# Kernel optimization log

Measured on AMD Instinct MI355X. Metric: run time of the kernel, lower is better.

The kernel has to match this reference:

```python
import jax, jax.numpy as jnp
import numpy as np

W_SEG = 2048   # segment length w
R = 4          # dilation rate
OFFSET = 0     # offset < r
H = 16         # num heads
C = 1024       # embed dim
M = W_SEG // R # tokens attended per segment


def _mha(xi, w_in, b_in, w_out, b_out):
    # xi: (b, s, m, c) -> causal multi-head self-attention per segment
    b, s, m, c = xi.shape
    dh = c // H
    qkv = jnp.einsum('bsmc,ec->bsme', xi, w_in) + b_in  # e = 3c
    q, k, v = jnp.split(qkv, 3, axis=-1)
    q = q.reshape(b, s, m, H, dh)
    k = k.reshape(b, s, m, H, dh)
    v = v.reshape(b, s, m, H, dh)
    scores = jnp.einsum('bsqhd,bskhd->bshqk', q, k) / jnp.sqrt(jnp.asarray(dh, xi.dtype))
    causal = jnp.tril(jnp.ones((m, m), dtype=bool))
    scores = jnp.where(causal, scores, jnp.asarray(-1e9, xi.dtype))
    p = jax.nn.softmax(scores, axis=-1)
    o = jnp.einsum('bshqk,bskhd->bsqhd', p, v).reshape(b, s, m, c)
    return jnp.einsum('bsmc,oc->bsmo', o, w_out) + b_out


def setup_inputs() -> dict:
    key = jax.random.key(0)
    k1, k2, k3, k4, k5 = jax.random.split(key, 5)
    x = jax.random.normal(k1, (4, 8192, C), dtype=jnp.float32)
    w_in = jax.random.normal(k2, (3 * C, C), dtype=jnp.float32) * (C ** -0.5)
    b_in = jnp.zeros((3 * C,), dtype=jnp.float32)
    w_out = jax.random.normal(k3, (C, C), dtype=jnp.float32) * (C ** -0.5)
    b_out = jnp.zeros((C,), dtype=jnp.float32)
    return {"x": x, "w_in": w_in, "b_in": b_in, "w_out": w_out, "b_out": b_out}


def reference(x, w_in, b_in, w_out, b_out):
    b, n, c = x.shape
    s = n // W_SEG  # number of segments
    xr = x.reshape(b, s, W_SEG, c)
    xi = xr[:, :, OFFSET::R, :]                # (b, s, m, c) dilated gather
    oi = _mha(xi, w_in, b_in, w_out, b_out)    # attention per segment
    out = jnp.zeros_like(xr).at[:, :, OFFSET::R, :].set(oi)  # scatter (disjoint indices)
    return out.reshape(b, n, c)
```

## Files before the change

kernel.cpp:

```cpp
#include <hip/hip_runtime.h>


typedef unsigned short u16;
typedef short short8 __attribute__((ext_vector_type(8)));
typedef short short4v __attribute__((ext_vector_type(4)));
typedef float f32x4 __attribute__((ext_vector_type(4)));

__device__ __forceinline__ u16 f2bf(float f) {
  unsigned u = __builtin_bit_cast(unsigned, f);
  u += 0x7FFFu + ((u >> 16) & 1u);
  return (u16)(u >> 16);
}

__device__ __forceinline__ void gload_lds16(const void* g, void* l) {
  __builtin_amdgcn_global_load_lds((const __attribute__((address_space(1))) void*)g,
                                   (__attribute__((address_space(3))) void*)l,
                                   16, 0, 0);
}

#define SBAR() asm volatile("s_barrier" ::: "memory")

__global__ void conv_gather(const float* __restrict__ x, u16* __restrict__ xi) {
  int t = blockIdx.x * 256 + threadIdx.x;
  if (t >= (8192 * 1024) / 8) return;
  int row = t >> 7;
  int col = (t & 127) << 3;
  size_t src = ((size_t)((row >> 9) << 11) + ((row & 511) << 2)) * 1024 + col;
  float4 v0 = *(const float4*)(x + src);
  float4 v1 = *(const float4*)(x + src + 4);
  short8 o;
  o[0] = f2bf(v0.x); o[1] = f2bf(v0.y); o[2] = f2bf(v0.z); o[3] = f2bf(v0.w);
  o[4] = f2bf(v1.x); o[5] = f2bf(v1.y); o[6] = f2bf(v1.z); o[7] = f2bf(v1.w);
  *(short8*)(xi + (size_t)row * 1024 + col) = o;
}

__global__ void conv_plain(const float* __restrict__ in, u16* __restrict__ out, int n8) {
  int t = blockIdx.x * 256 + threadIdx.x;
  if (t >= n8) return;
  size_t base = (size_t)t * 8;
  float4 v0 = *(const float4*)(in + base);
  float4 v1 = *(const float4*)(in + base + 4);
  short8 o;
  o[0] = f2bf(v0.x); o[1] = f2bf(v0.y); o[2] = f2bf(v0.z); o[3] = f2bf(v0.w);
  o[4] = f2bf(v1.x); o[5] = f2bf(v1.y); o[6] = f2bf(v1.z); o[7] = f2bf(v1.w);
  *(short8*)(out + base) = o;
}

template <int NCOLS, int MODE>
__global__ __launch_bounds__(512) void gemm_pipe(
    const u16* __restrict__ A, const u16* __restrict__ B,
    const float* __restrict__ bias, void* __restrict__ Cout) {
  constexpr int K = 1024, NT = 16, NTILE = NCOLS / 256;
  __shared__ u16 lds[3][24576];

  const int tid = threadIdx.x;
  const int w = tid >> 6, lane = tid & 63;
  const int wm = w >> 2, wn = w & 3;
  const int g = lane >> 4, lq = lane & 15;

  const int per = gridDim.x >> 3;
  const int s = (blockIdx.x & 7) * per + (blockIdx.x >> 3);
  const int m0 = (s / NTILE) * 128, n0 = (s % NTILE) * 256;

  const int srow = w * 8 + (lane >> 3);
  const int jch = (lane & 7) ^ ((lane >> 3) & 7);
  const u16* Ab = A + (size_t)(m0 + srow) * K + jch * 8;
  const u16* Bb = B + (size_t)(n0 + srow) * K + jch * 8;
  const int ldst = w * 512 + lane * 8;

#define SA(buf_, qd, kt) gload_lds16(Ab + (size_t)(qd) * 64 * K + (kt) * 64, &lds[buf_][(qd) * 4096 + ldst])
#define SB(buf_, qd, kt) gload_lds16(Bb + (size_t)(qd) * 64 * K + (kt) * 64, &lds[buf_][8192 + (qd) * 4096 + ldst])
#define STAGE6(kt)                                                                 \
  { const int nb_ = (kt) % 3;                                                      \
    SA(nb_, 0, kt); SA(nb_, 1, kt);                                                \
    SB(nb_, 0, kt); SB(nb_, 1, kt); SB(nb_, 2, kt); SB(nb_, 3, kt); }

  const int xw = lq & 7;
  const int arow = wm * 64 + lq;
  const int brow = wn * 64 + lq;

#define READ_TILE(aset, bset, tile_)                                               \
  { const int bufr = (tile_) % 3;                                                  \
    _Pragma("unroll") for (int kc = 0; kc < 2; ++kc) {                             \
      _Pragma("unroll") for (int mi = 0; mi < 4; ++mi)                             \
        aset[mi + 4 * kc] = *(const short8*)(                                      \
            &lds[bufr][(arow + mi * 16) * 64 + ((kc * 4 + g) ^ xw) * 8]);          \
      _Pragma("unroll") for (int ni = 0; ni < 4; ++ni)                             \
        bset[ni + 4 * kc] = *(const short8*)(                                      \
            &lds[bufr][8192 + (brow + ni * 16) * 64 + ((kc * 4 + g) ^ xw) * 8]);   \
    } }

#define MFMA_TILE(aset, bset)                                                      \
  __builtin_amdgcn_s_setprio(1);                                                   \
  _Pragma("unroll") for (int kc = 0; kc < 2; ++kc)                                 \
    _Pragma("unroll") for (int mi = 0; mi < 4; ++mi)                               \
      _Pragma("unroll") for (int ni = 0; ni < 4; ++ni)                             \
        acc[mi][ni] = __builtin_amdgcn_mfma_f32_16x16x32_bf16(                     \
            aset[mi + 4 * kc], bset[ni + 4 * kc], acc[mi][ni], 0, 0, 0);           \
  __builtin_amdgcn_s_setprio(0);

  f32x4 acc[4][4] = {};
  short8 aA[8], bA[8], aB[8], bB[8];

  STAGE6(0); STAGE6(1);
  asm volatile("s_waitcnt vmcnt(6)" ::: "memory");
  SBAR();
  READ_TILE(aA, bA, 0);

#pragma unroll 1
  for (int tt = 0; tt < NT; tt += 2) {
    if (tt + 2 < NT) STAGE6(tt + 2);
    if (tt + 2 < NT) { asm volatile("s_waitcnt vmcnt(6)" ::: "memory"); }
    else             { asm volatile("s_waitcnt vmcnt(0)" ::: "memory"); }
    asm volatile("s_waitcnt lgkmcnt(0)" ::: "memory");
    SBAR();
    READ_TILE(aB, bB, tt + 1);
    MFMA_TILE(aA, bA);

    if (tt + 3 < NT) STAGE6(tt + 3);
    if (tt + 3 < NT) { asm volatile("s_waitcnt vmcnt(6)" ::: "memory"); }
    else             { asm volatile("s_waitcnt vmcnt(0)" ::: "memory"); }
    asm volatile("s_waitcnt lgkmcnt(0)" ::: "memory");
    SBAR();
    if (tt + 2 < NT) READ_TILE(aA, bA, tt + 2);
    MFMA_TILE(aB, bB);
  }

  if (MODE == 0) {
    u16* C = (u16*)Cout;
    if (n0 < 2048) {
#pragma unroll
      for (int mi = 0; mi < 4; ++mi) {
#pragma unroll
        for (int ni = 0; ni < 4; ++ni) {
          const int col = n0 + wn * 64 + ni * 16 + lq;
          const float bv = bias[col];
          u16* dst = C + (size_t)(col >> 10) * 8388608 + (col & 1023);
#pragma unroll
          for (int r = 0; r < 4; ++r) {
            const int m = m0 + wm * 64 + mi * 16 + g * 4 + r;
            dst[(size_t)m * 1024] = f2bf(acc[mi][ni][r] + bv);
          }
        }
      }
    } else {
      u16* vt = C + 16777216;
#pragma unroll
      for (int mi = 0; mi < 4; ++mi) {
        const int m4 = m0 + wm * 64 + mi * 16 + g * 4;
        const int bs = m4 >> 9, k = m4 & 511;
#pragma unroll
        for (int ni = 0; ni < 4; ++ni) {
          const int cv = n0 - 2048 + wn * 64 + ni * 16 + lq;
          const int h = cv >> 6, d = cv & 63;
          const float bv = bias[cv + 2048];
          short4v pk;
#pragma unroll
          for (int r = 0; r < 4; ++r) pk[r] = (short)f2bf(acc[mi][ni][r] + bv);
          *(short4v*)(&vt[(size_t)((bs * 16 + h) * 64 + d) * 512 + k]) = pk;
        }
      }
    }
  } else {
    float* O = (float*)Cout;
#pragma unroll
    for (int mi = 0; mi < 4; ++mi) {
#pragma unroll
      for (int ni = 0; ni < 4; ++ni) {
        const int col = n0 + wn * 64 + ni * 16 + lq;
        const float bv = bias[col];
#pragma unroll
        for (int r = 0; r < 4; ++r) {
          const int m = m0 + wm * 64 + mi * 16 + g * 4 + r;
          const int orow = ((m >> 9) << 11) + ((m & 511) << 2);
          O[(size_t)orow * 1024 + col] = acc[mi][ni][r] + bv;
        }
      }
    }
    for (int i = 0; i < 48; ++i) {
      const int idx = i * 512 + tid;
      const int z = idx >> 13;
      const int mm = (idx & 8191) >> 6;
      const int ch = idx & 63;
      const int m = m0 + mm;
      const int orow = ((m >> 9) << 11) + ((m & 511) << 2) + 1 + z;
      *(float4*)(O + (size_t)orow * 1024 + n0 + ch * 4) =
          make_float4(0.f, 0.f, 0.f, 0.f);
    }
  }
#undef SA
#undef SB
#undef STAGE6
#undef READ_TILE
#undef MFMA_TILE
}

__global__ __launch_bounds__(512) void attn_kernel(const u16* __restrict__ qkv,
                                                   u16* __restrict__ o_ws) {
  __shared__ u16 Ks[512 * 64];
  __shared__ u16 Vs[64 * 512];
  __shared__ u16 Pl[8][16][40];

  const int tid = threadIdx.x;
  const int w = tid >> 6, lane = tid & 63;
  const int g = lane >> 4, lq = lane & 15;
  const int bh = blockIdx.x;
  const int bs = bh >> 4, h = bh & 15;

  const u16* baseq = qkv + (size_t)bs * 512 * 1024 + h * 64;
  const u16* basek = qkv + 8388608 + (size_t)bs * 512 * 1024 + h * 64;
  const u16* vhead = qkv + 16777216 + (size_t)bh * 32768;

  {
    const int rsub = lane >> 3;
    const int csw = (lane & 7) ^ rsub;
#pragma unroll
    for (int i = 0; i < 8; ++i) {
      const int step = i * 8 + w;
      gload_lds16(basek + (size_t)(step * 8 + rsub) * 1024 + csw * 8,
                  &Ks[step * 512 + lane * 8]);
    }
#pragma unroll
    for (int i = 0; i < 8; ++i) {
      const int d = i * 8 + w;
      gload_lds16(vhead + (size_t)d * 512 + (lane ^ (d & 7)) * 8,
                  &Vs[d * 512 + lane * 8]);
    }
  }
  __syncthreads();

  const int xw = lq & 7;
#pragma unroll 1
  for (int qi = 0; qi < 4; ++qi) {
    const int qt = ((qi & 1) ? (15 - w) : w) + (qi >> 1) * 16;
    const int q0 = qt * 16;
    const short8 qf0 = *(const short8*)(baseq + (size_t)(q0 + lq) * 1024 + g * 8);
    const short8 qf1 = *(const short8*)(baseq + (size_t)(q0 + lq) * 1024 + 32 + g * 8);
    f32x4 oacc[4] = {};
    float l_r[4] = {0.f, 0.f, 0.f, 0.f};
    const int nst = (qt + 2) >> 1;
#pragma unroll 1
    for (int kk = 0; kk < nst; ++kk) {
      const int kb = kk * 32;
      const bool last = (kk == nst - 1);
      f32x4 s[2];
#pragma unroll
      for (int tt = 0; tt < 2; ++tt) {
        const int r = kb + tt * 16 + lq;
        short8 klo = *(const short8*)(&Ks[r * 64 + ((g ^ xw) * 8)]);
        short8 khi = *(const short8*)(&Ks[r * 64 + (((4 + g) ^ xw) * 8)]);
        f32x4 z = {};
        z = __builtin_amdgcn_mfma_f32_16x16x32_bf16(qf0, klo, z, 0, 0, 0);
        z = __builtin_amdgcn_mfma_f32_16x16x32_bf16(qf1, khi, z, 0, 0, 0);
        s[tt] = z;
      }
#pragma unroll
      for (int tt = 0; tt < 2; ++tt) {
#pragma unroll
        for (int r = 0; r < 4; ++r) {
          float p = __expf(s[tt][r] * 0.125f);
          if (last && (kb + tt * 16 + lq > q0 + g * 4 + r)) p = 0.f;
          l_r[r] += p;
          Pl[w][g * 4 + r][tt * 16 + lq] = f2bf(p);
        }
      }
      short8 pf = *(const short8*)(&Pl[w][lq][g * 8]);
#pragma unroll
      for (int dt = 0; dt < 4; ++dt) {
        const int vr = dt * 16 + lq;
        short8 vf = *(const short8*)(&Vs[vr * 512 + ((((kb >> 3) + g) ^ xw) * 8)]);
        oacc[dt] = __builtin_amdgcn_mfma_f32_16x16x32_bf16(pf, vf, oacc[dt], 0, 0, 0);
      }
    }
#pragma unroll
    for (int r = 0; r < 4; ++r) {
      float l = l_r[r];
      l += __shfl_xor(l, 1);
      l += __shfl_xor(l, 2);
      l += __shfl_xor(l, 4);
      l += __shfl_xor(l, 8);
      const float inv = 1.0f / l;
      const int q = q0 + g * 4 + r;
      u16* dst = o_ws + (size_t)(bs * 512 + q) * 1024 + h * 64;
#pragma unroll
      for (int dt = 0; dt < 4; ++dt) dst[dt * 16 + lq] = f2bf(oacc[dt][r] * inv);
    }
  }
}

extern "C" void kernel_launch(void* const* d_in, const int* in_sizes, int n_in,
                              void* d_out, int out_size, void* d_ws, size_t ws_size,
                              hipStream_t stream) {
  const float* x     = (const float*)d_in[0];
  const float* w_in  = (const float*)d_in[1];
  const float* b_in  = (const float*)d_in[2];
  const float* w_out = (const float*)d_in[3];
  const float* b_out = (const float*)d_in[4];

  char* ws = (char*)d_ws;
  u16* xi_bf   = (u16*)(ws);
  u16* win_bf  = (u16*)(ws + 16777216);
  u16* wout_bf = (u16*)(ws + 16777216 + 6291456);
  u16* qkv     = (u16*)(ws + 16777216 + 6291456 + 2097152);
  u16* o_bf    = (u16*)(ws + 16777216 + 6291456 + 2097152 + 50331648);

  conv_gather<<<4096, 256, 0, stream>>>(x, xi_bf);
  conv_plain<<<1536, 256, 0, stream>>>(w_in, win_bf, (3072 * 1024) / 8);
  conv_plain<<<512, 256, 0, stream>>>(w_out, wout_bf, (1024 * 1024) / 8);
  gemm_pipe<3072, 0><<<768, 512, 0, stream>>>(xi_bf, win_bf, b_in, qkv);
  attn_kernel<<<256, 512, 0, stream>>>(qkv, o_bf);
  gemm_pipe<1024, 1><<<256, 512, 0, stream>>>(o_bf, wout_bf, b_out, d_out);
}
```

Baseline: 139.1 us.

## Use 256x256 QKV GEMM tiles with K=32 stages and fuse conversion kernels

The three fp32-to-bf16 conversion kernels are merged into one launch with block-index dispatch, which saves two launches. The QKV projection gets its own kernel with a 256x256 output tile, 32-wide K stages over 32 iterations and 8x4 MFMA accumulators per wave, halving the grid to 384 blocks. The larger tile raises operand reuse per load but doubles accumulator register pressure and may lower occupancy or leave CUs under-filled with fewer blocks.

```diff
diff --git a/kernel.cpp b/kernel.cpp
--- a/kernel.cpp
+++ b/kernel.cpp
@@ -20,47 +20,165 @@
 
 #define SBAR() asm volatile("s_barrier" ::: "memory")
 
-__global__ void conv_gather(const float* __restrict__ x, u16* __restrict__ xi) {
-  int t = blockIdx.x * 256 + threadIdx.x;
-  if (t >= (8192 * 1024) / 8) return;
-  int row = t >> 7;
-  int col = (t & 127) << 3;
-  size_t src = ((size_t)((row >> 9) << 11) + ((row & 511) << 2)) * 1024 + col;
-  float4 v0 = *(const float4*)(x + src);
-  float4 v1 = *(const float4*)(x + src + 4);
-  short8 o;
-  o[0] = f2bf(v0.x); o[1] = f2bf(v0.y); o[2] = f2bf(v0.z); o[3] = f2bf(v0.w);
-  o[4] = f2bf(v1.x); o[5] = f2bf(v1.y); o[6] = f2bf(v1.z); o[7] = f2bf(v1.w);
-  *(short8*)(xi + (size_t)row * 1024 + col) = o;
-}
-
-__global__ void conv_plain(const float* __restrict__ in, u16* __restrict__ out, int n8) {
-  int t = blockIdx.x * 256 + threadIdx.x;
-  if (t >= n8) return;
-  size_t base = (size_t)t * 8;
-  float4 v0 = *(const float4*)(in + base);
-  float4 v1 = *(const float4*)(in + base + 4);
-  short8 o;
-  o[0] = f2bf(v0.x); o[1] = f2bf(v0.y); o[2] = f2bf(v0.z); o[3] = f2bf(v0.w);
-  o[4] = f2bf(v1.x); o[5] = f2bf(v1.y); o[6] = f2bf(v1.z); o[7] = f2bf(v1.w);
-  *(short8*)(out + base) = o;
-}
-
-template <int NCOLS, int MODE>
-__global__ __launch_bounds__(512) void gemm_pipe(
+__global__ void conv_all(const float* __restrict__ x,
+                         const float* __restrict__ w_in,
+                         const float* __restrict__ w_out,
+                         u16* __restrict__ xi, u16* __restrict__ win,
+                         u16* __restrict__ wout) {
+  const int b = blockIdx.x;
+  if (b < 4096) {
+    int t = b * 256 + threadIdx.x;
+    int row = t >> 7;
+    int col = (t & 127) << 3;
+    size_t src = ((size_t)((row >> 9) << 11) + ((row & 511) << 2)) * 1024 + col;
+    float4 v0 = *(const float4*)(x + src);
+    float4 v1 = *(const float4*)(x + src + 4);
+    short8 o;
+    o[0] = f2bf(v0.x); o[1] = f2bf(v0.y); o[2] = f2bf(v0.z); o[3] = f2bf(v0.w);
+    o[4] = f2bf(v1.x); o[5] = f2bf(v1.y); o[6] = f2bf(v1.z); o[7] = f2bf(v1.w);
+    *(short8*)(xi + (size_t)row * 1024 + col) = o;
+  } else {
+    const float* src;
+    u16* dst;
+    int t;
+    if (b < 5632) { t = (b - 4096) * 256 + threadIdx.x; src = w_in;  dst = win; }
+    else          { t = (b - 5632) * 256 + threadIdx.x; src = w_out; dst = wout; }
+    size_t base = (size_t)t * 8;
+    float4 v0 = *(const float4*)(src + base);
+    float4 v1 = *(const float4*)(src + base + 4);
+    short8 o;
+    o[0] = f2bf(v0.x); o[1] = f2bf(v0.y); o[2] = f2bf(v0.z); o[3] = f2bf(v0.w);
+    o[4] = f2bf(v1.x); o[5] = f2bf(v1.y); o[6] = f2bf(v1.z); o[7] = f2bf(v1.w);
+    *(short8*)(dst + base) = o;
+  }
+}
+
+__global__ __launch_bounds__(512) void gemm_qkv32(
     const u16* __restrict__ A, const u16* __restrict__ B,
-    const float* __restrict__ bias, void* __restrict__ Cout) {
-  constexpr int K = 1024, NT = 16, NTILE = NCOLS / 256;
-  __shared__ u16 lds[3][24576];
+    const float* __restrict__ bias, u16* __restrict__ C) {
+  constexpr int K = 1024, NT = 32;
+  __shared__ u16 lds[3][16384];
 
   const int tid = threadIdx.x;
   const int w = tid >> 6, lane = tid & 63;
   const int wm = w >> 2, wn = w & 3;
   const int g = lane >> 4, lq = lane & 15;
 
+  const int s = (blockIdx.x & 7) * 48 + (blockIdx.x >> 3);
+  const int m0 = (s / 12) * 256, n0 = (s % 12) * 256;
+
+  const int r_ = tid >> 2;
+  const int jch = (tid & 3) ^ (r_ & 3) ^ ((r_ >> 2) & 3);
+  const u16* Ab = A + (size_t)(m0 + r_) * K + jch * 8;
+  const u16* Bb = B + (size_t)(n0 + r_) * K + jch * 8;
+
+#define SA32(buf_, q, kt) gload_lds16(Ab + (size_t)(q) * 128 * K + (kt) * 32, &lds[buf_][(q) * 4096 + tid * 8])
+#define SB32(buf_, q, kt) gload_lds16(Bb + (size_t)(q) * 128 * K + (kt) * 32, &lds[buf_][8192 + (q) * 4096 + tid * 8])
+#define STAGE4(kt)                                                                 \
+  { const int nb_ = (kt) % 3;                                                      \
+    SA32(nb_, 0, kt); SA32(nb_, 1, kt); SB32(nb_, 0, kt); SB32(nb_, 1, kt); }
+
+  const int xsw = ((lq & 3) ^ ((lq >> 2) & 3));
+  const int arow = wm * 128 + lq;
+  const int brow = wn * 64 + lq;
+  const int rch = (g ^ xsw) * 8;
+
+#define READ_T(aset, bset, tile_)                                                  \
+  { const int bufr = (tile_) % 3;                                                  \
+    _Pragma("unroll") for (int mi = 0; mi < 8; ++mi)                               \
+      aset[mi] = *(const short8*)(&lds[bufr][(arow + mi * 16) * 32 + rch]);        \
+    _Pragma("unroll") for (int ni = 0; ni < 4; ++ni)                               \
+      bset[ni] = *(const short8*)(&lds[bufr][8192 + (brow + ni * 16) * 32 + rch]); }
+
+#define MFMA_T(aset, bset)                                                         \
+  __builtin_amdgcn_s_setprio(1);                                                   \
+  _Pragma("unroll") for (int mi = 0; mi < 8; ++mi)                                 \
+    _Pragma("unroll") for (int ni = 0; ni < 4; ++ni)                               \
+      acc[mi][ni] = __builtin_amdgcn_mfma_f32_16x16x32_bf16(                       \
+          aset[mi], bset[ni], acc[mi][ni], 0, 0, 0);                               \
+  __builtin_amdgcn_s_setprio(0);
+
+  f32x4 acc[8][4] = {};
+  short8 aA[8], bA[4], aB[8], bB[4];
+
+  STAGE4(0); STAGE4(1);
+  asm volatile("s_waitcnt vmcnt(4)" ::: "memory");
+  SBAR();
+  READ_T(aA, bA, 0);
+
+#pragma unroll 1
+  for (int tt = 0; tt < NT; tt += 2) {
+    if (tt + 2 < NT) STAGE4(tt + 2);
+    if (tt + 2 < NT) { asm volatile("s_waitcnt vmcnt(4)" ::: "memory"); }
+    else             { asm volatile("s_waitcnt vmcnt(0)" ::: "memory"); }
+    asm volatile("s_waitcnt lgkmcnt(0)" ::: "memory");
+    SBAR();
+    READ_T(aB, bB, tt + 1);
+    MFMA_T(aA, bA);
+
+    if (tt + 3 < NT) STAGE4(tt + 3);
+    if (tt + 3 < NT) { asm volatile("s_waitcnt vmcnt(4)" ::: "memory"); }
+    else             { asm volatile("s_waitcnt vmcnt(0)" ::: "memory"); }
+    asm volatile("s_waitcnt lgkmcnt(0)" ::: "memory");
+    SBAR();
+    if (tt + 2 < NT) READ_T(aA, bA, tt + 2);
+    MFMA_T(aB, bB);
+  }
+
+  if (n0 < 2048) {
+#pragma unroll
+    for (int mi = 0; mi < 8; ++mi) {
+#pragma unroll
+      for (int ni = 0; ni < 4; ++ni) {
+        const int col = n0 + wn * 64 + ni * 16 + lq;
+        const float bv = bias[col];
+        u16* dst = C + (size_t)(col >> 10) * 8388608 + (col & 1023);
+#pragma unroll
+        for (int r = 0; r < 4; ++r) {
+          const int m = m0 + wm * 128 + mi * 16 + g * 4 + r;
+          dst[(size_t)m * 1024] = f2bf(acc[mi][ni][r] + bv);
+        }
+      }
+    }
+  } else {
+    u16* vt = C + 16777216;
+#pragma unroll
+    for (int mi = 0; mi < 8; ++mi) {
+      const int m4 = m0 + wm * 128 + mi * 16 + g * 4;
+      const int bs = m4 >> 9, k = m4 & 511;
+#pragma unroll
+      for (int ni = 0; ni < 4; ++ni) {
+        const int cv = n0 - 2048 + wn * 64 + ni * 16 + lq;
+        const int h = cv >> 6, d = cv & 63;
+        const float bv = bias[cv + 2048];
+        short4v pk;
+#pragma unroll
+        for (int r = 0; r < 4; ++r) pk[r] = (short)f2bf(acc[mi][ni][r] + bv);
+        *(short4v*)(&vt[(size_t)((bs * 16 + h) * 64 + d) * 512 + k]) = pk;
+      }
+    }
+  }
+#undef SA32
+#undef SB32
+#undef STAGE4
+#undef READ_T
+#undef MFMA_T
+}
+
+__global__ __launch_bounds__(512) void gemm_out(
+    const u16* __restrict__ A, const u16* __restrict__ B,
+    const float* __restrict__ bias, float* __restrict__ O) {
+  constexpr int K = 1024, NT = 16;
+  __shared__ u16 lds[3][24576];
+
+  const int tid = threadIdx.x;
+  const int w = tid >> 6, lane = tid & 63;
+  const int wm = w >> 2, wn = w & 3;
+  const int g = lane >> 4, lq = lane & 15;
+
   const int per = gridDim.x >> 3;
   const int s = (blockIdx.x & 7) * per + (blockIdx.x >> 3);
-  const int m0 = (s / NTILE) * 128, n0 = (s % NTILE) * 256;
+  const int m0 = (s >> 2) * 128, n0 = (s & 3) * 256;
 
   const int srow = w * 8 + (lane >> 3);
   const int jch = (lane & 7) ^ ((lane >> 3) & 7);
@@ -126,67 +244,29 @@
     MFMA_TILE(aB, bB);
   }
 
-  if (MODE == 0) {
-    u16* C = (u16*)Cout;
-    if (n0 < 2048) {
-#pragma unroll
-      for (int mi = 0; mi < 4; ++mi) {
-#pragma unroll
-        for (int ni = 0; ni < 4; ++ni) {
-          const int col = n0 + wn * 64 + ni * 16 + lq;
-          const float bv = bias[col];
-          u16* dst = C + (size_t)(col >> 10) * 8388608 + (col & 1023);
-#pragma unroll
-          for (int r = 0; r < 4; ++r) {
-            const int m = m0 + wm * 64 + mi * 16 + g * 4 + r;
-            dst[(size_t)m * 1024] = f2bf(acc[mi][ni][r] + bv);
-          }
-        }
-      }
-    } else {
-      u16* vt = C + 16777216;
-#pragma unroll
-      for (int mi = 0; mi < 4; ++mi) {
-        const int m4 = m0 + wm * 64 + mi * 16 + g * 4;
-        const int bs = m4 >> 9, k = m4 & 511;
-#pragma unroll
-        for (int ni = 0; ni < 4; ++ni) {
-          const int cv = n0 - 2048 + wn * 64 + ni * 16 + lq;
-          const int h = cv >> 6, d = cv & 63;
-          const float bv = bias[cv + 2048];
-          short4v pk;
-#pragma unroll
-          for (int r = 0; r < 4; ++r) pk[r] = (short)f2bf(acc[mi][ni][r] + bv);
-          *(short4v*)(&vt[(size_t)((bs * 16 + h) * 64 + d) * 512 + k]) = pk;
-        }
-      }
-    }
-  } else {
-    float* O = (float*)Cout;
-#pragma unroll
-    for (int mi = 0; mi < 4; ++mi) {
-#pragma unroll
-      for (int ni = 0; ni < 4; ++ni) {
-        const int col = n0 + wn * 64 + ni * 16 + lq;
-        const float bv = bias[col];
-#pragma unroll
-        for (int r = 0; r < 4; ++r) {
-          const int m = m0 + wm * 64 + mi * 16 + g * 4 + r;
-          const int orow = ((m >> 9) << 11) + ((m & 511) << 2);
-          O[(size_t)orow * 1024 + col] = acc[mi][ni][r] + bv;
-        }
-      }
-    }
-    for (int i = 0; i < 48; ++i) {
-      const int idx = i * 512 + tid;
-      const int z = idx >> 13;
-      const int mm = (idx & 8191) >> 6;
-      const int ch = idx & 63;
-      const int m = m0 + mm;
-      const int orow = ((m >> 9) << 11) + ((m & 511) << 2) + 1 + z;
-      *(float4*)(O + (size_t)orow * 1024 + n0 + ch * 4) =
-          make_float4(0.f, 0.f, 0.f, 0.f);
-    }
+#pragma unroll
+  for (int mi = 0; mi < 4; ++mi) {
+#pragma unroll
+    for (int ni = 0; ni < 4; ++ni) {
+      const int col = n0 + wn * 64 + ni * 16 + lq;
+      const float bv = bias[col];
+#pragma unroll
+      for (int r = 0; r < 4; ++r) {
+        const int m = m0 + wm * 64 + mi * 16 + g * 4 + r;
+        const int orow = ((m >> 9) << 11) + ((m & 511) << 2);
+        O[(size_t)orow * 1024 + col] = acc[mi][ni][r] + bv;
+      }
+    }
+  }
+  for (int i = 0; i < 48; ++i) {
+    const int idx = i * 512 + tid;
+    const int z = idx >> 13;
+    const int mm = (idx & 8191) >> 6;
+    const int ch = idx & 63;
+    const int m = m0 + mm;
+    const int orow = ((m >> 9) << 11) + ((m & 511) << 2) + 1 + z;
+    *(float4*)(O + (size_t)orow * 1024 + n0 + ch * 4) =
+        make_float4(0.f, 0.f, 0.f, 0.f);
   }
 #undef SA
 #undef SB
@@ -304,10 +384,8 @@
   u16* qkv     = (u16*)(ws + 16777216 + 6291456 + 2097152);
   u16* o_bf    = (u16*)(ws + 16777216 + 6291456 + 2097152 + 50331648);
 
-  conv_gather<<<4096, 256, 0, stream>>>(x, xi_bf);
-  conv_plain<<<1536, 256, 0, stream>>>(w_in, win_bf, (3072 * 1024) / 8);
-  conv_plain<<<512, 256, 0, stream>>>(w_out, wout_bf, (1024 * 1024) / 8);
-  gemm_pipe<3072, 0><<<768, 512, 0, stream>>>(xi_bf, win_bf, b_in, qkv);
+  conv_all<<<6144, 256, 0, stream>>>(x, w_in, w_out, xi_bf, win_bf, wout_bf);
+  gemm_qkv32<<<384, 512, 0, stream>>>(xi_bf, win_bf, b_in, qkv);
   attn_kernel<<<256, 512, 0, stream>>>(qkv, o_bf);
-  gemm_pipe<1024, 1><<<256, 512, 0, stream>>>(o_bf, wout_bf, b_out, d_out);
-}
+  gemm_out<<<256, 512, 0, stream>>>(o_bf, wout_bf, b_out, (float*)d_out);
+}
```

Result: slower. 146.9 us (+5.6%).
